# Kernel tuning notes

Measured on AMD Instinct MI355X. Metric: run time of the kernel, lower is better.

## Reference

```python
import jax, jax.numpy as jnp
import numpy as np

EPS = 1e-8
NUM_SHIFTS = 3


def setup_inputs() -> dict:
    key = jax.random.key(0)
    ks = jax.random.split(key, 12)
    B, N, D, C = 64, 8192, 128, 256
    memory = jax.random.normal(ks[0], (B, N, D), dtype=jnp.float32)
    controller_state = jax.random.normal(ks[1], (B, C), dtype=jnp.float32)
    pw = jax.random.uniform(ks[2], (B, N), dtype=jnp.float32)
    previous_weights = pw / jnp.sum(pw, axis=-1, keepdims=True)
    glorot = jax.nn.initializers.glorot_uniform()
    Wk = glorot(ks[3], (C, D), jnp.float32)
    Wb = glorot(ks[4], (C, 1), jnp.float32)
    bb = jnp.zeros((1,), jnp.float32)
    Wg = glorot(ks[5], (C, 1), jnp.float32)
    bg = jnp.zeros((1,), jnp.float32)
    Ws = glorot(ks[6], (C, NUM_SHIFTS), jnp.float32)
    bs = jnp.zeros((NUM_SHIFTS,), jnp.float32)
    Wgam = glorot(ks[7], (C, 1), jnp.float32)
    bgam = jnp.ones((1,), jnp.float32)  # sharpening_bias = 1.0
    return {"memory": memory, "controller_state": controller_state,
            "previous_weights": previous_weights, "Wk": Wk, "Wb": Wb, "bb": bb,
            "Wg": Wg, "bg": bg, "Ws": Ws, "bs": bs, "Wgam": Wgam, "bgam": bgam}


def _circular_convolution(w, s):
    # w: (B, N) weights, s: (B, K) shift kernel over offsets -K//2..K//2
    K = s.shape[-1]
    offsets = np.arange(K) - K // 2
    out = jnp.zeros_like(w)
    for k in range(K):  # K is tiny (3)
        out = out + s[:, k:k + 1] * jnp.roll(w, int(offsets[k]), axis=-1)
    return out


def reference(memory, controller_state, previous_weights,
              Wk, Wb, bb, Wg, bg, Ws, bs, Wgam, bgam):
    # content addressing
    key = controller_state @ Wk                                   # (B, D)
    beta = jax.nn.softplus(controller_state @ Wb + bb) + 1.0      # (B, 1)
    dot = jnp.einsum('bd,bnd->bn', key, memory)                   # (B, N)
    key_norm = jnp.linalg.norm(key, axis=-1, keepdims=True)       # (B, 1)
    mem_norm = jnp.linalg.norm(memory, axis=-1)                   # (B, N)
    similarity = dot / (key_norm * mem_norm + EPS)
    content_weights = jax.nn.softmax(beta * similarity, axis=-1)
    # interpolation gate
    gate = jax.nn.sigmoid(controller_state @ Wg + bg)             # (B, 1)
    gated = gate * content_weights + (1.0 - gate) * previous_weights
    # location addressing: circular shift
    shift_kernel = jax.nn.softmax(controller_state @ Ws + bs, axis=-1)
    shifted = _circular_convolution(gated, shift_kernel)
    # sharpening
    gamma = jax.nn.softplus(controller_state @ Wgam + bgam) + 1.0  # (B, 1)
    sharpened = jnp.power(shifted + 1e-8, gamma)
    weights = sharpened / (jnp.sum(sharpened, axis=-1, keepdims=True) + EPS)
    return weights
```

## Files before the change

### kernel.cpp

```cpp
#include <hip/hip_runtime.h>
#include <math.h>

#define BB 64
#define NN 8192
#define DD 128
#define CC 256
#define EPSF 1e-8f
#define ROWS 128

__device__ inline float softplusf(float x) {
    return fmaxf(x, 0.f) + log1pf(expf(-fabsf(x)));
}

__global__ __launch_bounds__(128)
void head_small(const float* __restrict__ cs,
                const float* __restrict__ Wk,
                const float* __restrict__ Wb, const float* __restrict__ bb,
                const float* __restrict__ Wg, const float* __restrict__ bg,
                const float* __restrict__ Ws, const float* __restrict__ bs,
                const float* __restrict__ Wgam, const float* __restrict__ bgam,
                float* __restrict__ key_out, float* __restrict__ scal_out) {
    const int b = blockIdx.x;
    const int t = threadIdx.x;
    __shared__ float s_cs[CC];
    __shared__ float s_red[2];

    for (int c = t; c < CC; c += 128) s_cs[c] = cs[b * CC + c];
    __syncthreads();

    float kacc = 0.f;
    #pragma unroll 8
    for (int c = 0; c < CC; ++c) kacc = fmaf(s_cs[c], Wk[c * DD + t], kacc);
    key_out[b * DD + t] = kacc;

    float a0 = 0.f, a1 = 0.f, a2 = 0.f, a3 = 0.f, a4 = 0.f, a5 = 0.f;
    for (int c = t; c < CC; c += 128) {
        float x = s_cs[c];
        a0 = fmaf(x, Wb[c], a0);
        a1 = fmaf(x, Wg[c], a1);
        a2 = fmaf(x, Ws[c * 3 + 0], a2);
        a3 = fmaf(x, Ws[c * 3 + 1], a3);
        a4 = fmaf(x, Ws[c * 3 + 2], a4);
        a5 = fmaf(x, Wgam[c], a5);
    }

    float vals[7] = { kacc * kacc, a0, a1, a2, a3, a4, a5 };
    float outv[7];
    const int wid = t >> 6, lane = t & 63;
    for (int k = 0; k < 7; ++k) {
        float v = vals[k];
        for (int off = 32; off > 0; off >>= 1) v += __shfl_down(v, off);
        __syncthreads();
        if (lane == 0) s_red[wid] = v;
        __syncthreads();
        outv[k] = s_red[0] + s_red[1];
    }

    if (t == 0) {
        float key_norm = sqrtf(outv[0]);
        float beta  = softplusf(outv[1] + bb[0]) + 1.f;
        float gate  = 1.f / (1.f + expf(-(outv[2] + bg[0])));
        float sh0 = outv[3] + bs[0], sh1 = outv[4] + bs[1], sh2 = outv[5] + bs[2];
        float m = fmaxf(sh0, fmaxf(sh1, sh2));
        float e0 = expf(sh0 - m), e1 = expf(sh1 - m), e2 = expf(sh2 - m);
        float inv = 1.f / (e0 + e1 + e2);
        float gamma = softplusf(outv[6] + bgam[0]) + 1.f;
        float* s = scal_out + b * 8;
        s[0] = beta; s[1] = gate; s[2] = gamma;
        s[3] = e0 * inv; s[4] = e1 * inv; s[5] = e2 * inv;
        s[6] = key_norm; s[7] = 0.f;
    }
}

__global__ __launch_bounds__(256)
void head_dot(const float* __restrict__ mem,
              const float* __restrict__ key, const float* __restrict__ scal,
              float* __restrict__ out) {
    const int b = blockIdx.y;
    const int chunk = blockIdx.x * ROWS;
    const int t = threadIdx.x;
    const int g = t >> 5;
    const int l = t & 31;

    const float4 k4 = ((const float4*)(key + b * DD))[l];
    const float beta = scal[b * 8 + 0];
    const float key_norm = scal[b * 8 + 6];
    const float* base = mem + (size_t)b * NN * DD;

    #pragma unroll 4
    for (int i = 0; i < ROWS / 8; ++i) {
        const int row = chunk + i * 8 + g;
        const float4 v = ((const float4*)(base + (size_t)row * DD))[l];
        float dot = v.x * k4.x + v.y * k4.y + v.z * k4.z + v.w * k4.w;
        float nr  = v.x * v.x + v.y * v.y + v.z * v.z + v.w * v.w;
        #pragma unroll
        for (int off = 16; off > 0; off >>= 1) {
            dot += __shfl_xor(dot, off, 32);
            nr  += __shfl_xor(nr,  off, 32);
        }
        if (l == 0) {
            float mem_norm = sqrtf(nr);
            float sim = dot / (key_norm * mem_norm + EPSF);
            out[(size_t)b * NN + row] = beta * sim;
        }
    }
}

__device__ inline float blockReduceSum1024(float v, float* red) {
    for (int off = 32; off > 0; off >>= 1) v += __shfl_down(v, off);
    const int wid = threadIdx.x >> 6, lane = threadIdx.x & 63;
    __syncthreads();
    if (lane == 0) red[wid] = v;
    __syncthreads();
    if (wid == 0) {
        float r = (lane < 16) ? red[lane] : 0.f;
        for (int off = 8; off > 0; off >>= 1) r += __shfl_down(r, off);
        if (lane == 0) red[0] = r;
    }
    __syncthreads();
    return red[0];
}

__device__ inline float blockReduceMax1024(float v, float* red) {
    for (int off = 32; off > 0; off >>= 1) v = fmaxf(v, __shfl_down(v, off));
    const int wid = threadIdx.x >> 6, lane = threadIdx.x & 63;
    __syncthreads();
    if (lane == 0) red[wid] = v;
    __syncthreads();
    if (wid == 0) {
        float r = (lane < 16) ? red[lane] : -INFINITY;
        for (int off = 8; off > 0; off >>= 1) r = fmaxf(r, __shfl_down(r, off));
        if (lane == 0) red[0] = r;
    }
    __syncthreads();
    return red[0];
}

__global__ __launch_bounds__(1024)
void head_finish(const float* __restrict__ prev,
                 const float* __restrict__ scal, float* __restrict__ out) {
    const int b = blockIdx.x;
    const int t = threadIdx.x;
    __shared__ float w[NN];
    __shared__ float red[16];

    const float gate  = scal[b * 8 + 1];
    const float gamma = scal[b * 8 + 2];
    const float s0 = scal[b * 8 + 3], s1 = scal[b * 8 + 4], s2 = scal[b * 8 + 5];

    float lmax = -INFINITY;
    #pragma unroll
    for (int j = 0; j < NN / 1024; ++j) {
        const int i = t + j * 1024;
        const float v = out[(size_t)b * NN + i];
        w[i] = v;
        lmax = fmaxf(lmax, v);
    }
    const float gmax = blockReduceMax1024(lmax, red);

    float lsum = 0.f;
    #pragma unroll
    for (int j = 0; j < NN / 1024; ++j) {
        const int i = t + j * 1024;
        const float e = expf(w[i] - gmax);
        w[i] = e;
        lsum += e;
    }
    const float gsum = blockReduceSum1024(lsum, red);
    const float invs = 1.f / gsum;

    #pragma unroll
    for (int j = 0; j < NN / 1024; ++j) {
        const int i = t + j * 1024;
        const float cw = w[i] * invs;
        w[i] = gate * cw + (1.f - gate) * prev[(size_t)b * NN + i];
    }
    __syncthreads();

    float sharp[NN / 1024];
    float lps = 0.f;
    #pragma unroll
    for (int j = 0; j < NN / 1024; ++j) {
        const int i = t + j * 1024;
        const float sh = s0 * w[(i + 1) & (NN - 1)] + s1 * w[i] + s2 * w[(i - 1) & (NN - 1)];
        const float p = powf(sh + 1e-8f, gamma);
        sharp[j] = p;
        lps += p;
    }
    const float gps = blockReduceSum1024(lps, red);
    const float invp = 1.f / (gps + EPSF);

    #pragma unroll
    for (int j = 0; j < NN / 1024; ++j) {
        out[(size_t)b * NN + t + j * 1024] = sharp[j] * invp;
    }
}

extern "C" void kernel_launch(void* const* d_in, const int* in_sizes, int n_in,
                              void* d_out, int out_size, void* d_ws, size_t ws_size,
                              hipStream_t stream) {
    const float* mem  = (const float*)d_in[0];
    const float* cs   = (const float*)d_in[1];
    const float* prev = (const float*)d_in[2];
    const float* Wk   = (const float*)d_in[3];
    const float* Wb   = (const float*)d_in[4];
    const float* bb   = (const float*)d_in[5];
    const float* Wg   = (const float*)d_in[6];
    const float* bg   = (const float*)d_in[7];
    const float* Ws   = (const float*)d_in[8];
    const float* bs   = (const float*)d_in[9];
    const float* Wgam = (const float*)d_in[10];
    const float* bgam = (const float*)d_in[11];
    float* out = (float*)d_out;

    float* key  = (float*)d_ws;
    float* scal = key + BB * DD;

    head_small<<<BB, 128, 0, stream>>>(cs, Wk, Wb, bb, Wg, bg, Ws, bs,
                                       Wgam, bgam, key, scal);
    dim3 gridB(NN / ROWS, BB);
    head_dot<<<gridB, 256, 0, stream>>>(mem, key, scal, out);
    head_finish<<<BB, 1024, 0, stream>>>(prev, scal, out);
}
```

Baseline: 415.6 us.

## Use 16-lane row groups in dot kernel and vectorize finish kernel I/O

The dot kernel now assigns each row to 16 lanes that load two float4 values each. This shortens the shuffle reduction and lets each wavefront handle four rows at a time. Per-row results are staged in shared memory so each block writes one coalesced run instead of scattered single-lane stores. The finish kernel reads scores and previous weights as float4 and writes its output through shared memory as float4 stores, at the cost of extra syncs and shared-memory traffic. The unroll factor of the key projection loop is also raised.

Result: faster. 407.5 us (-2.0%).

```diff
diff --git a/kernel.cpp b/kernel.cpp
--- a/kernel.cpp
+++ b/kernel.cpp
@@ -29,7 +29,7 @@
     __syncthreads();
 
     float kacc = 0.f;
-    #pragma unroll 8
+    #pragma unroll 16
     for (int c = 0; c < CC; ++c) kacc = fmaf(s_cs[c], Wk[c * DD + t], kacc);
     key_out[b * DD + t] = kacc;
 
@@ -79,31 +79,41 @@
     const int b = blockIdx.y;
     const int chunk = blockIdx.x * ROWS;
     const int t = threadIdx.x;
-    const int g = t >> 5;
-    const int l = t & 31;
-
-    const float4 k4 = ((const float4*)(key + b * DD))[l];
+    const int w = t >> 6;
+    const int l = t & 63;
+    const int sub = l >> 4;
+    const int sl = l & 15;
+
+    const float4 k0 = ((const float4*)(key + b * DD))[sl];
+    const float4 k1 = ((const float4*)(key + b * DD))[sl + 16];
     const float beta = scal[b * 8 + 0];
     const float key_norm = scal[b * 8 + 6];
     const float* base = mem + (size_t)b * NN * DD;
 
-    #pragma unroll 4
-    for (int i = 0; i < ROWS / 8; ++i) {
-        const int row = chunk + i * 8 + g;
-        const float4 v = ((const float4*)(base + (size_t)row * DD))[l];
-        float dot = v.x * k4.x + v.y * k4.y + v.z * k4.z + v.w * k4.w;
-        float nr  = v.x * v.x + v.y * v.y + v.z * v.z + v.w * v.w;
+    __shared__ float s_res[ROWS];
+
+    #pragma unroll
+    for (int i = 0; i < ROWS / 16; ++i) {
+        const int row = chunk + i * 16 + w * 4 + sub;
+        const float4* rp = (const float4*)(base + (size_t)row * DD);
+        const float4 v0 = rp[sl];
+        const float4 v1 = rp[sl + 16];
+        float dot = v0.x * k0.x + v0.y * k0.y + v0.z * k0.z + v0.w * k0.w
+                  + v1.x * k1.x + v1.y * k1.y + v1.z * k1.z + v1.w * k1.w;
+        float nr  = v0.x * v0.x + v0.y * v0.y + v0.z * v0.z + v0.w * v0.w
+                  + v1.x * v1.x + v1.y * v1.y + v1.z * v1.z + v1.w * v1.w;
         #pragma unroll
-        for (int off = 16; off > 0; off >>= 1) {
-            dot += __shfl_xor(dot, off, 32);
-            nr  += __shfl_xor(nr,  off, 32);
+        for (int off = 8; off > 0; off >>= 1) {
+            dot += __shfl_xor(dot, off);
+            nr  += __shfl_xor(nr,  off);
         }
-        if (l == 0) {
-            float mem_norm = sqrtf(nr);
-            float sim = dot / (key_norm * mem_norm + EPSF);
-            out[(size_t)b * NN + row] = beta * sim;
+        if (sl == 0) {
+            const float sim = dot / (key_norm * sqrtf(nr) + EPSF);
+            s_res[i * 16 + w * 4 + sub] = beta * sim;
         }
     }
+    __syncthreads();
+    if (t < ROWS) out[(size_t)b * NN + chunk + t] = s_res[t];
 }
 
 __device__ inline float blockReduceSum1024(float v, float* red) {
@@ -148,13 +158,17 @@
     const float gamma = scal[b * 8 + 2];
     const float s0 = scal[b * 8 + 3], s1 = scal[b * 8 + 4], s2 = scal[b * 8 + 5];
 
+    const float4* out4  = (const float4*)(out  + (size_t)b * NN);
+    const float4* prev4 = (const float4*)(prev + (size_t)b * NN);
+    float4* w4 = (float4*)w;
+
     float lmax = -INFINITY;
     #pragma unroll
-    for (int j = 0; j < NN / 1024; ++j) {
-        const int i = t + j * 1024;
-        const float v = out[(size_t)b * NN + i];
-        w[i] = v;
-        lmax = fmaxf(lmax, v);
+    for (int j = 0; j < NN / 4096; ++j) {
+        const int i4 = t + j * 1024;
+        const float4 v = out4[i4];
+        w4[i4] = v;
+        lmax = fmaxf(lmax, fmaxf(fmaxf(v.x, v.y), fmaxf(v.z, v.w)));
     }
     const float gmax = blockReduceMax1024(lmax, red);
 
@@ -170,10 +184,15 @@
     const float invs = 1.f / gsum;
 
     #pragma unroll
-    for (int j = 0; j < NN / 1024; ++j) {
-        const int i = t + j * 1024;
-        const float cw = w[i] * invs;
-        w[i] = gate * cw + (1.f - gate) * prev[(size_t)b * NN + i];
+    for (int j = 0; j < NN / 4096; ++j) {
+        const int i4 = t + j * 1024;
+        const float4 p = prev4[i4];
+        float4 c = w4[i4];
+        c.x = gate * c.x * invs + (1.f - gate) * p.x;
+        c.y = gate * c.y * invs + (1.f - gate) * p.y;
+        c.z = gate * c.z * invs + (1.f - gate) * p.z;
+        c.w = gate * c.w * invs + (1.f - gate) * p.w;
+        w4[i4] = c;
     }
     __syncthreads();
 
@@ -190,9 +209,15 @@
     const float gps = blockReduceSum1024(lps, red);
     const float invp = 1.f / (gps + EPSF);
 
-    #pragma unroll
-    for (int j = 0; j < NN / 1024; ++j) {
-        out[(size_t)b * NN + t + j * 1024] = sharp[j] * invp;
+    __syncthreads();
+    #pragma unroll
+    for (int j = 0; j < NN / 1024; ++j) w[t + j * 1024] = sharp[j] * invp;
+    __syncthreads();
+    float4* o4 = (float4*)(out + (size_t)b * NN);
+    #pragma unroll
+    for (int j = 0; j < NN / 4096; ++j) {
+        const int i4 = t + j * 1024;
+        o4[i4] = w4[i4];
     }
 }
 
```
